# Kernel optimization log

Hardware: AMD Instinct MI355X
Metric: run time of the kernel (lower is better)

Reference implementation:

```python
import jax, jax.numpy as jnp
import numpy as np

B, S, D = 4, 2048, 1024
H, HD = 16, 64
DFF = 4096
EPS = 1e-6


def setup_inputs() -> dict:
    key = jax.random.key(0)
    ks = jax.random.split(key, 16)
    sc = 0.02
    def w(k, shape):
        return jax.random.normal(k, shape, dtype=jnp.float32) * sc
    return {
        'x': jax.random.normal(ks[0], (B, S, D), dtype=jnp.float32),
        'wq': w(ks[1], (D, D)), 'bq': jnp.zeros((D,), jnp.float32),
        'wk': w(ks[2], (D, D)), 'bk': jnp.zeros((D,), jnp.float32),
        'wv': w(ks[3], (D, D)), 'bv': jnp.zeros((D,), jnp.float32),
        'wo': w(ks[4], (D, D)), 'bo': jnp.zeros((D,), jnp.float32),
        'w1': w(ks[5], (D, DFF)), 'b1': jnp.zeros((DFF,), jnp.float32),
        'w2': w(ks[6], (DFF, D)), 'b2': jnp.zeros((D,), jnp.float32),
        'ln1_a': jnp.ones((D,), jnp.float32), 'ln1_b': jnp.zeros((D,), jnp.float32),
        'ln2_a': jnp.ones((D,), jnp.float32), 'ln2_b': jnp.zeros((D,), jnp.float32),
    }


def layernorm(x, alpha, bias):
    # Matches torch module: std is unbiased (ddof=1), divide by (std + eps)
    mean = jnp.mean(x, axis=-1, keepdims=True)
    var = jnp.sum((x - mean) ** 2, axis=-1, keepdims=True) / (x.shape[-1] - 1)
    std = jnp.sqrt(var)
    return alpha * ((x - mean) / (std + EPS)) + bias


def mha(x, wq, bq, wk, bk, wv, bv, wo, bo):
    q = (x @ wq + bq).reshape(B, S, H, HD)
    k = (x @ wk + bk).reshape(B, S, H, HD)
    v = (x @ wv + bv).reshape(B, S, H, HD)
    scores = jnp.einsum('bqhd,bkhd->bhqk', q, k) / jnp.sqrt(jnp.float32(HD))
    attn = jax.nn.softmax(scores, axis=-1)
    out = jnp.einsum('bhqk,bkhd->bqhd', attn, v).reshape(B, S, D)
    return out @ wo + bo


def reference(x, wq, bq, wk, bk, wv, bv, wo, bo, w1, b1, w2, b2,
              ln1_a, ln1_b, ln2_a, ln2_b):
    # Residual 1: x + MHA(LN(x))   (dropout = identity, eval mode)
    x = x + mha(layernorm(x, ln1_a, ln1_b), wq, bq, wk, bk, wv, bv, wo, bo)
    # Residual 2: x + FFN(LN(x))
    h = layernorm(x, ln2_a, ln2_b)
    ffn = jax.nn.relu(h @ w1 + b1) @ w2 + b2
    return x + ffn
```

## Files before the change

kernel.cpp:

```cpp
#include <hip/hip_runtime.h>

#define S_ 2048
#define D_ 1024

typedef unsigned short u16;
typedef unsigned int u32;
typedef __bf16 bf16x8 __attribute__((ext_vector_type(8)));
typedef unsigned short us8 __attribute__((ext_vector_type(8)));
typedef unsigned short us4 __attribute__((ext_vector_type(4)));
typedef unsigned int u32x4 __attribute__((ext_vector_type(4)));
typedef float f32x4 __attribute__((ext_vector_type(4)));

#if __has_builtin(__builtin_amdgcn_exp2f)
#define EXP2(x) __builtin_amdgcn_exp2f(x)
#else
#define EXP2(x) exp2f(x)
#endif

static __device__ __forceinline__ u16 f2bf(float f) {
  unsigned u = __builtin_bit_cast(unsigned, f);
  u += 0x7fffu + ((u >> 16) & 1u);
  return (u16)(u >> 16);
}

static __device__ __forceinline__ unsigned cvtpk_bf16(float lo, float hi) {
  unsigned r;
  asm("v_cvt_pk_bf16_f32 %0, %1, %2" : "=v"(r) : "v"(lo), "v"(hi));
  return r;
}

static __device__ __forceinline__ f32x4 mfma16(bf16x8 a, bf16x8 b, f32x4 c) {
  return __builtin_amdgcn_mfma_f32_16x16x32_bf16(a, b, c, 0, 0, 0);
}

static __device__ __forceinline__ void gload16(const void* g, void* lds) {
  __builtin_amdgcn_global_load_lds((const __attribute__((address_space(1))) void*)g,
                                   (__attribute__((address_space(3))) void*)lds, 16, 0, 0);
}

__global__ __launch_bounds__(256) void wtrans_kernel(const float* __restrict__ in,
                                                     u16* __restrict__ out, int K, int N,
                                                     float scale) {
  __shared__ float t[32][33];
  const int n0 = blockIdx.x * 32, k0 = blockIdx.y * 32;
  const int tx = threadIdx.x, ty = threadIdx.y;
#pragma unroll
  for (int i = 0; i < 4; i++)
    t[ty + 8 * i][tx] = in[(size_t)(k0 + ty + 8 * i) * N + n0 + tx];
  __syncthreads();
#pragma unroll
  for (int i = 0; i < 4; i++)
    out[(size_t)(n0 + ty + 8 * i) * K + k0 + tx] = f2bf(t[tx][ty + 8 * i] * scale);
}

__global__ __launch_bounds__(256) void bcat_kernel(const float* __restrict__ bq,
                                                   const float* __restrict__ bk,
                                                   const float* __restrict__ bv,
                                                   float* __restrict__ out, float qs) {
  const int i = blockIdx.x * 256 + threadIdx.x;
  out[i] = (i < 1024) ? bq[i] * qs : ((i < 2048) ? bk[i - 1024] : bv[i - 2048]);
}

__global__ __launch_bounds__(256) void ln_kernel(const float* __restrict__ in,
                                                 u16* __restrict__ out,
                                                 const float* __restrict__ alpha,
                                                 const float* __restrict__ beta) {
  const int row = blockIdx.x;
  const int tid = threadIdx.x;
  const float4 v = *(const float4*)(in + (size_t)row * D_ + tid * 4);
  float s = v.x + v.y + v.z + v.w;
  float ss = v.x * v.x + v.y * v.y + v.z * v.z + v.w * v.w;
#pragma unroll
  for (int off = 32; off >= 1; off >>= 1) {
    s += __shfl_xor(s, off);
    ss += __shfl_xor(ss, off);
  }
  __shared__ float red[8];
  const int w = tid >> 6, lane = tid & 63;
  if (lane == 0) { red[w] = s; red[4 + w] = ss; }
  __syncthreads();
  s = red[0] + red[1] + red[2] + red[3];
  ss = red[4] + red[5] + red[6] + red[7];
  const float mean = s * (1.0f / D_);
  const float var = (ss - s * mean) * (1.0f / (D_ - 1));
  const float inv = 1.0f / (sqrtf(var) + 1e-6f);
  const int j = tid * 4;
  const float4 av = *(const float4*)(alpha + j);
  const float4 bv = *(const float4*)(beta + j);
  us4 o;
  o[0] = f2bf((v.x - mean) * inv * av.x + bv.x);
  o[1] = f2bf((v.y - mean) * inv * av.y + bv.y);
  o[2] = f2bf((v.z - mean) * inv * av.z + bv.z);
  o[3] = f2bf((v.w - mean) * inv * av.w + bv.w);
  *(us4*)(out + (size_t)row * D_ + j) = o;
}

template <int OM, bool RELU, bool RESID>
__global__ __launch_bounds__(512, 2) void gemm_bt(const u16* __restrict__ A,
                                                  const u16* __restrict__ Bt,
                                                  const float* __restrict__ bias,
                                                  const float* __restrict__ resid,
                                                  void* __restrict__ outp,
                                                  void* __restrict__ out1,
                                                  void* __restrict__ out2, int N, int K) {
  __shared__ u16 lds[3 * 24576];
  const int tid = threadIdx.x;
  const int lane = tid & 63, w = tid >> 6;
  const int g = lane >> 4, r = lane & 15;
  const int wr = w >> 1, wc = w & 1;

  const int gx = gridDim.x;
  const int nwg = gx * gridDim.y;
  const int orig = blockIdx.y * gx + blockIdx.x;
  const int nid = (orig & 7) * (nwg >> 3) + (orig >> 3);
  const int bx = nid % gx, by = nid / gx;
  const size_t row0 = (size_t)by * 256;
  const int col0 = bx * 128;

  float bias4[4];
#pragma unroll
  for (int n = 0; n < 4; n++) bias4[n] = bias[col0 + wc * 64 + n * 16 + r];

  f32x4 acc[4][4];
#pragma unroll
  for (int m = 0; m < 4; m++)
#pragma unroll
    for (int n = 0; n < 4; n++) {
      f32x4 z = {bias4[n], bias4[n], bias4[n], bias4[n]};
      acc[m][n] = z;
    }

  const int lrow = w * 8 + (lane >> 3);
  const int scol = 8 * ((lane & 7) ^ (lane >> 3));
  const u16* gA = A + (row0 + lrow) * (size_t)K + scol;
  const u16* gB = Bt + ((size_t)col0 + lrow) * (size_t)K + scol;
  const int nt = K >> 6;
  const int sw = (r & 7) << 3;

  int bufi = 0;
#pragma unroll
  for (int t0 = 0; t0 < 2; t0++) {
    u16* dA = lds + t0 * 24576 + w * 512;
#pragma unroll
    for (int j = 0; j < 4; j++) gload16(gA + (size_t)(j * 64) * K + t0 * 64, dA + j * 4096);
#pragma unroll
    for (int j = 0; j < 2; j++)
      gload16(gB + (size_t)(j * 64) * K + t0 * 64, dA + 16384 + j * 4096);
  }

  for (int t = 0; t < nt; ++t) {
    if (t + 1 < nt)
      asm volatile("s_waitcnt vmcnt(6)" ::: "memory");
    else
      asm volatile("s_waitcnt vmcnt(0)" ::: "memory");
    __builtin_amdgcn_s_barrier();
    asm volatile("" ::: "memory");
    const bool st = (t + 2 < nt);
    const int bn = (bufi + 2 >= 3) ? bufi - 1 : bufi + 2;
    u16* dS = lds + bn * 24576 + w * 512;
    const size_t ko = (size_t)(t + 2) * 64;
    const u16* As_ = lds + bufi * 24576;
    const u16* Bs_ = As_ + 16384;
    bf16x8 bfr[2][4];

#pragma unroll
    for (int p = 0; p < 4; ++p) {
      bf16x8 a0 = __builtin_bit_cast(
          bf16x8, *(const us8*)(As_ + (wr * 64 + p * 16 + r) * 64 + ((g * 8) ^ sw)));
      bf16x8 a1 = __builtin_bit_cast(
          bf16x8, *(const us8*)(As_ + (wr * 64 + p * 16 + r) * 64 + ((32 + g * 8) ^ sw)));
      if (p == 0) {
#pragma unroll
        for (int kk = 0; kk < 2; kk++)
#pragma unroll
          for (int n = 0; n < 4; n++)
            bfr[kk][n] = __builtin_bit_cast(
                bf16x8,
                *(const us8*)(Bs_ + (wc * 64 + n * 16 + r) * 64 + ((kk * 32 + g * 8) ^ sw)));
      }
      if (st) {
        if (p == 0) {
          gload16(gA + ko, dS);
          gload16(gA + (size_t)64 * K + ko, dS + 4096);
        } else if (p == 1) {
          gload16(gA + (size_t)128 * K + ko, dS + 8192);
          gload16(gA + (size_t)192 * K + ko, dS + 12288);
        } else if (p == 2) {
          gload16(gB + ko, dS + 16384);
          gload16(gB + (size_t)64 * K + ko, dS + 20480);
        }
      }
      asm volatile("s_waitcnt lgkmcnt(0)" ::: "memory");
      __builtin_amdgcn_sched_barrier(0);
      __builtin_amdgcn_s_setprio(1);
#pragma unroll
      for (int n = 0; n < 4; n++) {
        acc[p][n] = mfma16(a0, bfr[0][n], acc[p][n]);
        acc[p][n] = mfma16(a1, bfr[1][n], acc[p][n]);
      }
      __builtin_amdgcn_s_setprio(0);
      if (p < 3) __builtin_amdgcn_s_barrier();
    }
    bufi = (bufi == 2) ? 0 : bufi + 1;
  }

#pragma unroll
  for (int m = 0; m < 4; m++)
#pragma unroll
    for (int n = 0; n < 4; n++) {
      if (OM == 2) {
        const int seg = col0 >> 10;
        const int cl = (col0 & 1023) + wc * 64 + n * 16 + r;
        if (seg == 2) {
          const int head = cl >> 6, hd = cl & 63;
          const size_t rg0 = row0 + wr * 64 + m * 16 + 4 * g;
          const int b = (int)(rg0 >> 11), s0 = (int)(rg0 & 2047);
          us4 o;
#pragma unroll
          for (int i = 0; i < 4; i++) o[i] = f2bf(acc[m][n][i]);
          *(us4*)((u16*)out2 + (((size_t)(b * 16 + head) * 64 + hd) * S_ + s0)) = o;
        } else {
          u16* dst = (u16*)(seg == 0 ? outp : out1);
#pragma unroll
          for (int i = 0; i < 4; i++) {
            const size_t rg = row0 + wr * 64 + m * 16 + 4 * g + i;
            dst[rg * D_ + cl] = f2bf(acc[m][n][i]);
          }
        }
      } else {
#pragma unroll
        for (int i = 0; i < 4; i++) {
          const size_t rg = row0 + wr * 64 + m * 16 + 4 * g + i;
          const int cg = col0 + wc * 64 + n * 16 + r;
          float v = acc[m][n][i];
          if (RESID) v += resid[rg * N + cg];
          if (RELU) v = fmaxf(v, 0.0f);
          if (OM == 1)
            ((float*)outp)[rg * N + cg] = v;
          else
            ((u16*)outp)[rg * N + cg] = f2bf(v);
        }
      }
    }
}

template <bool RELU>
__global__ __launch_bounds__(512, 2) void gemm_bt256(const u16* __restrict__ A,
                                                     const u16* __restrict__ Bt,
                                                     const float* __restrict__ bias,
                                                     u16* __restrict__ outp, int N, int K) {
  __shared__ u16 lds[2 * 32768];
  const int tid = threadIdx.x;
  const int lane = tid & 63, w = tid >> 6;
  const int g = lane >> 4, r = lane & 15;
  const int wr = w >> 2, wc = w & 3;
  const int gx = gridDim.x;
  const int nwg = gx * gridDim.y;
  const int orig = blockIdx.y * gx + blockIdx.x;
  const int nid = (orig & 7) * (nwg >> 3) + (orig >> 3);
  const int bx = nid % gx, by = nid / gx;
  const size_t row0 = (size_t)by * 256;
  const int col0 = bx * 256;

  float bias4[4];
#pragma unroll
  for (int n = 0; n < 4; n++) bias4[n] = bias[col0 + wc * 64 + n * 16 + r];

  f32x4 acc[8][4];
#pragma unroll
  for (int m = 0; m < 8; m++)
#pragma unroll
    for (int n = 0; n < 4; n++) {
      f32x4 z = {bias4[n], bias4[n], bias4[n], bias4[n]};
      acc[m][n] = z;
    }

  const int lrow = tid >> 3;
  const int scol = 8 * ((tid & 7) ^ (lrow & 7));
  const u16* gA = A + (row0 + lrow) * (size_t)K + scol;
  const u16* gB = Bt + ((size_t)col0 + lrow) * (size_t)K + scol;
  const int nt = K >> 6;
  const int sw = (r & 7) << 3;

  {
    u16* d = lds + w * 512;
#pragma unroll
    for (int j = 0; j < 4; j++) gload16(gA + (size_t)(j * 64) * K, d + j * 4096);
#pragma unroll
    for (int j = 0; j < 4; j++) gload16(gB + (size_t)(j * 64) * K, d + 16384 + j * 4096);
  }

  for (int t = 0; t < nt; ++t) {
    const u16* As_ = lds + (t & 1) * 32768;
    const u16* Bs_ = As_ + 16384;
    if (t + 1 < nt) {
      u16* d = lds + ((t + 1) & 1) * 32768 + w * 512;
      const size_t ko = (size_t)(t + 1) * 64;
#pragma unroll
      for (int j = 0; j < 4; j++) gload16(gA + (size_t)(j * 64) * K + ko, d + j * 4096);
#pragma unroll
      for (int j = 0; j < 4; j++) gload16(gB + (size_t)(j * 64) * K + ko, d + 16384 + j * 4096);
      asm volatile("s_waitcnt vmcnt(8)" ::: "memory");
    } else {
      asm volatile("s_waitcnt vmcnt(0)" ::: "memory");
    }
    __builtin_amdgcn_s_barrier();
    asm volatile("" ::: "memory");

    bf16x8 bfr[2][4];
#pragma unroll
    for (int kk = 0; kk < 2; kk++)
#pragma unroll
      for (int n = 0; n < 4; n++)
        bfr[kk][n] = __builtin_bit_cast(
            bf16x8, *(const us8*)(Bs_ + (wc * 64 + n * 16 + r) * 64 + ((kk * 32 + g * 8) ^ sw)));

#pragma unroll
    for (int p = 0; p < 4; ++p) {
      bf16x8 af[2][2];
#pragma unroll
      for (int mm = 0; mm < 2; mm++) {
        const int row = wr * 128 + (p * 2 + mm) * 16 + r;
        af[0][mm] = __builtin_bit_cast(bf16x8, *(const us8*)(As_ + row * 64 + ((g * 8) ^ sw)));
        af[1][mm] =
            __builtin_bit_cast(bf16x8, *(const us8*)(As_ + row * 64 + ((32 + g * 8) ^ sw)));
      }
      asm volatile("" ::: "memory");
      if (p > 0) __builtin_amdgcn_s_barrier();
      asm volatile("s_waitcnt lgkmcnt(0)" ::: "memory");
      __builtin_amdgcn_sched_barrier(0);
      __builtin_amdgcn_s_setprio(1);
#pragma unroll
      for (int mm = 0; mm < 2; mm++)
#pragma unroll
        for (int n = 0; n < 4; n++) {
          acc[p * 2 + mm][n] = mfma16(af[0][mm], bfr[0][n], acc[p * 2 + mm][n]);
          acc[p * 2 + mm][n] = mfma16(af[1][mm], bfr[1][n], acc[p * 2 + mm][n]);
        }
      __builtin_amdgcn_s_setprio(0);
    }
    asm volatile("" ::: "memory");
    __builtin_amdgcn_s_barrier();
  }

#pragma unroll
  for (int m = 0; m < 8; m++)
#pragma unroll
    for (int n = 0; n < 4; n++)
#pragma unroll
      for (int i = 0; i < 4; i++) {
        const size_t rg = row0 + wr * 128 + m * 16 + 4 * g + i;
        const int cg = col0 + wc * 64 + n * 16 + r;
        float v = acc[m][n][i];
        if (RELU) v = fmaxf(v, 0.0f);
        outp[rg * N + cg] = f2bf(v);
      }
}

__global__ __launch_bounds__(256) void attn_kernel(const u16* __restrict__ Q,
                                                   const u16* __restrict__ Km,
                                                   const u16* __restrict__ Vt_g,
                                                   u16* __restrict__ O) {
  __shared__ u16 Klds[64 * 64];
  __shared__ u16 Vlds[64 * 68];
  const int tid = threadIdx.x;
  const int lane = tid & 63, w = tid >> 6;
  const int g = lane >> 4, r = lane & 15;
  const int bh = blockIdx.y;
  const int b = bh >> 4, head = bh & 15;
  const size_t rowbase = (size_t)b * S_;
  const int colbase = head * 64;
  const int qw = blockIdx.x * 128 + w * 32;

  bf16x8 qf0[2], qf1[2];
#pragma unroll
  for (int qh = 0; qh < 2; qh++) {
    const u16* qrow = Q + (rowbase + qw + qh * 16 + r) * D_ + colbase;
    qf0[qh] = __builtin_bit_cast(bf16x8, *(const us8*)(qrow + g * 8));
    qf1[qh] = __builtin_bit_cast(bf16x8, *(const us8*)(qrow + 32 + g * 8));
  }

  const int srow = tid >> 3;
  const int sslot = (tid & 7) ^ (srow & 7);
  const u16* Kg = Km + (rowbase + srow) * D_ + colbase + sslot * 8;
  const u16* Vg = Vt_g + ((size_t)bh * 64 + srow) * S_ + (tid & 7) * 8;
  char* lK = (char*)Klds + w * 1024;

  const us8 onesw = {0x3F80, 0x3F80, 0x3F80, 0x3F80, 0x3F80, 0x3F80, 0x3F80, 0x3F80};
  const bf16x8 ones8 = __builtin_bit_cast(bf16x8, onesw);

  f32x4 lacc[2];
  f32x4 oacc[2][4];
#pragma unroll
  for (int qh = 0; qh < 2; qh++) {
    f32x4 z = {0.0f, 0.0f, 0.0f, 0.0f};
    lacc[qh] = z;
#pragma unroll
    for (int n = 0; n < 4; n++) oacc[qh][n] = z;
  }

  for (int kt = 0; kt < S_ / 64; kt++) {
    const us8 v0 = *(const us8*)(Vg + (size_t)kt * 64);
    const us8 v1 = *(const us8*)(Vg + 32 * S_ + (size_t)kt * 64);
    __syncthreads();
    gload16(Kg + (size_t)kt * 64 * D_, lK);
    gload16(Kg + (size_t)(kt * 64 + 32) * D_, lK + 4096);
    *(us8*)(Vlds + srow * 68 + (tid & 7) * 8) = v0;
    *(us8*)(Vlds + (srow + 32) * 68 + (tid & 7) * 8) = v1;
    __syncthreads();

    f32x4 st[4][2];
    __builtin_amdgcn_s_setprio(1);
#pragma unroll
    for (int f = 0; f < 4; f++) {
      const int row = f * 16 + r;
      const int sw = row & 7;
      const bf16x8 k0 = __builtin_bit_cast(bf16x8, *(const us8*)(Klds + row * 64 + (g ^ sw) * 8));
      const bf16x8 k1 =
          __builtin_bit_cast(bf16x8, *(const us8*)(Klds + row * 64 + ((g + 4) ^ sw) * 8));
#pragma unroll
      for (int qh = 0; qh < 2; qh++) {
        f32x4 z = {0.0f, 0.0f, 0.0f, 0.0f};
        st[f][qh] = mfma16(k0, qf0[qh], z);
        st[f][qh] = mfma16(k1, qf1[qh], st[f][qh]);
      }
    }
    __builtin_amdgcn_s_setprio(0);
    u32 pw[2][8];
#pragma unroll
    for (int qh = 0; qh < 2; qh++)
#pragma unroll
      for (int f = 0; f < 4; f++) {
        const float e0 = EXP2(st[f][qh][0]);
        const float e1 = EXP2(st[f][qh][1]);
        const float e2 = EXP2(st[f][qh][2]);
        const float e3 = EXP2(st[f][qh][3]);
        pw[qh][f * 2] = cvtpk_bf16(e0, e1);
        pw[qh][f * 2 + 1] = cvtpk_bf16(e2, e3);
      }

    bf16x8 a0[2], a1[2];
#pragma unroll
    for (int qh = 0; qh < 2; qh++) {
      const u32x4 a0w = {pw[qh][0], pw[qh][1], pw[qh][2], pw[qh][3]};
      const u32x4 a1w = {pw[qh][4], pw[qh][5], pw[qh][6], pw[qh][7]};
      a0[qh] = __builtin_bit_cast(bf16x8, a0w);
      a1[qh] = __builtin_bit_cast(bf16x8, a1w);
    }
    __builtin_amdgcn_s_setprio(1);
#pragma unroll
    for (int qh = 0; qh < 2; qh++) {
      lacc[qh] = mfma16(a0[qh], ones8, lacc[qh]);
      lacc[qh] = mfma16(a1[qh], ones8, lacc[qh]);
    }
#pragma unroll
    for (int n = 0; n < 4; n++) {
      const u16* vr = Vlds + (n * 16 + r) * 68;
      const us4 v00 = *(const us4*)(vr + g * 4);
      const us4 v01 = *(const us4*)(vr + 16 + g * 4);
      const us4 v10 = *(const us4*)(vr + 32 + g * 4);
      const us4 v11 = *(const us4*)(vr + 48 + g * 4);
      const bf16x8 vb0 =
          __builtin_bit_cast(bf16x8, __builtin_shufflevector(v00, v01, 0, 1, 2, 3, 4, 5, 6, 7));
      const bf16x8 vb1 =
          __builtin_bit_cast(bf16x8, __builtin_shufflevector(v10, v11, 0, 1, 2, 3, 4, 5, 6, 7));
#pragma unroll
      for (int qh = 0; qh < 2; qh++) {
        oacc[qh][n] = mfma16(a0[qh], vb0, oacc[qh][n]);
        oacc[qh][n] = mfma16(a1[qh], vb1, oacc[qh][n]);
      }
    }
    __builtin_amdgcn_s_setprio(0);
  }

#pragma unroll
  for (int qh = 0; qh < 2; qh++) {
    float ld[4];
#pragma unroll
    for (int i = 0; i < 4; i++) ld[i] = 1.0f / lacc[qh][i];
#pragma unroll
    for (int n = 0; n < 4; n++)
#pragma unroll
      for (int i = 0; i < 4; i++)
        O[(rowbase + qw + qh * 16 + 4 * g + i) * D_ + colbase + n * 16 + r] =
            f2bf(oacc[qh][n][i] * ld[i]);
  }
}

extern "C" void kernel_launch(void* const* d_in, const int* in_sizes, int n_in, void* d_out,
                              int out_size, void* d_ws, size_t ws_size, hipStream_t stream) {
  (void)in_sizes; (void)n_in; (void)out_size; (void)ws_size;
  const float* x = (const float*)d_in[0];
  const float* wq = (const float*)d_in[1];
  const float* bq = (const float*)d_in[2];
  const float* wk = (const float*)d_in[3];
  const float* bk = (const float*)d_in[4];
  const float* wv = (const float*)d_in[5];
  const float* bv = (const float*)d_in[6];
  const float* wo = (const float*)d_in[7];
  const float* bo = (const float*)d_in[8];
  const float* w1 = (const float*)d_in[9];
  const float* b1 = (const float*)d_in[10];
  const float* w2 = (const float*)d_in[11];
  const float* b2 = (const float*)d_in[12];
  const float* ln1a = (const float*)d_in[13];
  const float* ln1b = (const float*)d_in[14];
  const float* ln2a = (const float*)d_in[15];
  const float* ln2b = (const float*)d_in[16];

  char* ws = (char*)d_ws;
  const size_t MB = 1ull << 20;
  u16* wqkv = (u16*)(ws + 0 * MB);
  u16* wqt = wqkv;
  u16* wkt = (u16*)(ws + 2 * MB);
  u16* wvt = (u16*)(ws + 4 * MB);
  u16* wot = (u16*)(ws + 6 * MB);
  u16* w1t = (u16*)(ws + 8 * MB);
  u16* w2t = (u16*)(ws + 16 * MB);
  u16* xA = (u16*)(ws + 24 * MB);
  u16* qb = (u16*)(ws + 40 * MB);
  u16* kb = (u16*)(ws + 56 * MB);
  u16* vt = (u16*)(ws + 72 * MB);
  float* bcat = (float*)(ws + 88 * MB);
  u16* ff1 = (u16*)(ws + 40 * MB);
  float* x1 = (float*)(ws + 104 * MB);

  const float QSCALE = 0.125f * 1.4426950408889634f;

  const dim3 tb(32, 8);
  wtrans_kernel<<<dim3(32, 32), tb, 0, stream>>>(wq, wqt, 1024, 1024, QSCALE);
  wtrans_kernel<<<dim3(32, 32), tb, 0, stream>>>(wk, wkt, 1024, 1024, 1.0f);
  wtrans_kernel<<<dim3(32, 32), tb, 0, stream>>>(wv, wvt, 1024, 1024, 1.0f);
  wtrans_kernel<<<dim3(32, 32), tb, 0, stream>>>(wo, wot, 1024, 1024, 1.0f);
  wtrans_kernel<<<dim3(128, 32), tb, 0, stream>>>(w1, w1t, 1024, 4096, 1.0f);
  wtrans_kernel<<<dim3(32, 128), tb, 0, stream>>>(w2, w2t, 4096, 1024, 1.0f);
  bcat_kernel<<<12, 256, 0, stream>>>(bq, bk, bv, bcat, QSCALE);

  ln_kernel<<<8192, 256, 0, stream>>>(x, xA, ln1a, ln1b);
  gemm_bt<2, false, false><<<dim3(24, 32), 512, 0, stream>>>(xA, wqkv, bcat, nullptr, qb, kb, vt,
                                                             3072, 1024);
  attn_kernel<<<dim3(16, 64), 256, 0, stream>>>(qb, kb, vt, xA);
  gemm_bt<1, false, true><<<dim3(8, 32), 512, 0, stream>>>(xA, wot, bo, x, x1, nullptr, nullptr,
                                                           1024, 1024);
  ln_kernel<<<8192, 256, 0, stream>>>(x1, xA, ln2a, ln2b);
  gemm_bt256<true><<<dim3(16, 32), 512, 0, stream>>>(xA, w1t, b1, ff1, 4096, 1024);
  gemm_bt<1, false, true><<<dim3(8, 32), 512, 0, stream>>>(ff1, w2t, b2, x1, (float*)d_out,
                                                           nullptr, nullptr, 1024, 4096);
}
```

Before: 381.6 us.

## Double-buffer K/V tiles in attention and merge weight prep kernels

The attention kernel now double-buffers K and V tiles in LDS. The next tile's global loads are issued before the current tile's QK and PV MFMAs, and one barrier per iteration replaces two. Separately, the six weight-transpose launches and the bias-concat launch are folded into a single prep kernel to cut launch overhead. The cost is double the LDS use in attention, which may lower occupancy, plus a full vmcnt/lgkmcnt wait at the end of each iteration.

```diff
diff --git a/kernel.cpp b/kernel.cpp
--- a/kernel.cpp
+++ b/kernel.cpp
@@ -38,27 +38,44 @@
                                    (__attribute__((address_space(3))) void*)lds, 16, 0, 0);
 }
 
-__global__ __launch_bounds__(256) void wtrans_kernel(const float* __restrict__ in,
-                                                     u16* __restrict__ out, int K, int N,
-                                                     float scale) {
+__global__ __launch_bounds__(256) void prep_kernel(
+    const float* __restrict__ wq, const float* __restrict__ wk, const float* __restrict__ wv,
+    const float* __restrict__ wo, const float* __restrict__ w1, const float* __restrict__ w2,
+    const float* __restrict__ bq, const float* __restrict__ bk, const float* __restrict__ bv,
+    u16* __restrict__ wqkv, u16* __restrict__ wot, u16* __restrict__ w1t,
+    u16* __restrict__ w2t, float* __restrict__ bcat, float qs) {
+  const int bid = blockIdx.x;
+  const int tx = threadIdx.x, ty = threadIdx.y;
+  if (bid >= 12288) {
+    const int i = (bid - 12288) * 256 + ty * 32 + tx;
+    bcat[i] = (i < 1024) ? bq[i] * qs : ((i < 2048) ? bk[i - 1024] : bv[i - 2048]);
+    return;
+  }
+  const float* in;
+  u16* out;
+  int K, N, idx;
+  float sc = 1.0f;
+  if (bid < 4096) {
+    K = 1024; N = 1024; idx = bid & 1023;
+    if (bid < 1024)      { in = wq; out = wqkv;             sc = qs; }
+    else if (bid < 2048) { in = wk; out = wqkv + (1 << 20); }
+    else if (bid < 3072) { in = wv; out = wqkv + (2 << 20); }
+    else                 { in = wo; out = wot; }
+  } else if (bid < 8192) {
+    in = w1; out = w1t; K = 1024; N = 4096; idx = bid - 4096;
+  } else {
+    in = w2; out = w2t; K = 4096; N = 1024; idx = bid - 8192;
+  }
+  const int nb = N >> 5;
+  const int n0 = (idx % nb) * 32, k0 = (idx / nb) * 32;
   __shared__ float t[32][33];
-  const int n0 = blockIdx.x * 32, k0 = blockIdx.y * 32;
-  const int tx = threadIdx.x, ty = threadIdx.y;
 #pragma unroll
   for (int i = 0; i < 4; i++)
     t[ty + 8 * i][tx] = in[(size_t)(k0 + ty + 8 * i) * N + n0 + tx];
   __syncthreads();
 #pragma unroll
   for (int i = 0; i < 4; i++)
-    out[(size_t)(n0 + ty + 8 * i) * K + k0 + tx] = f2bf(t[tx][ty + 8 * i] * scale);
-}
-
-__global__ __launch_bounds__(256) void bcat_kernel(const float* __restrict__ bq,
-                                                   const float* __restrict__ bk,
-                                                   const float* __restrict__ bv,
-                                                   float* __restrict__ out, float qs) {
-  const int i = blockIdx.x * 256 + threadIdx.x;
-  out[i] = (i < 1024) ? bq[i] * qs : ((i < 2048) ? bk[i - 1024] : bv[i - 2048]);
+    out[(size_t)(n0 + ty + 8 * i) * K + k0 + tx] = f2bf(t[tx][ty + 8 * i] * sc);
 }
 
 __global__ __launch_bounds__(256) void ln_kernel(const float* __restrict__ in,
@@ -361,8 +378,8 @@
                                                    const u16* __restrict__ Km,
                                                    const u16* __restrict__ Vt_g,
                                                    u16* __restrict__ O) {
-  __shared__ u16 Klds[64 * 64];
-  __shared__ u16 Vlds[64 * 68];
+  __shared__ u16 Klds[2 * 4096];
+  __shared__ u16 Vlds[2 * 4352];
   const int tid = threadIdx.x;
   const int lane = tid & 63, w = tid >> 6;
   const int g = lane >> 4, r = lane & 15;
@@ -384,7 +401,6 @@
   const int sslot = (tid & 7) ^ (srow & 7);
   const u16* Kg = Km + (rowbase + srow) * D_ + colbase + sslot * 8;
   const u16* Vg = Vt_g + ((size_t)bh * 64 + srow) * S_ + (tid & 7) * 8;
-  char* lK = (char*)Klds + w * 1024;
 
   const us8 onesw = {0x3F80, 0x3F80, 0x3F80, 0x3F80, 0x3F80, 0x3F80, 0x3F80, 0x3F80};
   const bf16x8 ones8 = __builtin_bit_cast(bf16x8, onesw);
@@ -399,15 +415,29 @@
     for (int n = 0; n < 4; n++) oacc[qh][n] = z;
   }
 
+  {
+    const us8 pv0 = *(const us8*)(Vg);
+    const us8 pv1 = *(const us8*)(Vg + 32 * S_);
+    gload16(Kg, (char*)Klds + w * 1024);
+    gload16(Kg + (size_t)32 * D_, (char*)Klds + w * 1024 + 4096);
+    *(us8*)(Vlds + srow * 68 + (tid & 7) * 8) = pv0;
+    *(us8*)(Vlds + (srow + 32) * 68 + (tid & 7) * 8) = pv1;
+    __syncthreads();
+  }
+
   for (int kt = 0; kt < S_ / 64; kt++) {
-    const us8 v0 = *(const us8*)(Vg + (size_t)kt * 64);
-    const us8 v1 = *(const us8*)(Vg + 32 * S_ + (size_t)kt * 64);
-    __syncthreads();
-    gload16(Kg + (size_t)kt * 64 * D_, lK);
-    gload16(Kg + (size_t)(kt * 64 + 32) * D_, lK + 4096);
-    *(us8*)(Vlds + srow * 68 + (tid & 7) * 8) = v0;
-    *(us8*)(Vlds + (srow + 32) * 68 + (tid & 7) * 8) = v1;
-    __syncthreads();
+    const int cur = kt & 1, nxt = cur ^ 1;
+    const bool more = (kt + 1 < S_ / 64);
+    us8 nv0, nv1;
+    if (more) {
+      nv0 = *(const us8*)(Vg + (size_t)(kt + 1) * 64);
+      nv1 = *(const us8*)(Vg + 32 * S_ + (size_t)(kt + 1) * 64);
+      gload16(Kg + (size_t)(kt + 1) * 64 * D_, (char*)Klds + nxt * 8192 + w * 1024);
+      gload16(Kg + (size_t)((kt + 1) * 64 + 32) * D_,
+              (char*)Klds + nxt * 8192 + w * 1024 + 4096);
+    }
+    const u16* Kc = Klds + cur * 4096;
+    const u16* Vc = Vlds + cur * 4352;
 
     f32x4 st[4][2];
     __builtin_amdgcn_s_setprio(1);
@@ -415,9 +445,9 @@
     for (int f = 0; f < 4; f++) {
       const int row = f * 16 + r;
       const int sw = row & 7;
-      const bf16x8 k0 = __builtin_bit_cast(bf16x8, *(const us8*)(Klds + row * 64 + (g ^ sw) * 8));
+      const bf16x8 k0 = __builtin_bit_cast(bf16x8, *(const us8*)(Kc + row * 64 + (g ^ sw) * 8));
       const bf16x8 k1 =
-          __builtin_bit_cast(bf16x8, *(const us8*)(Klds + row * 64 + ((g + 4) ^ sw) * 8));
+          __builtin_bit_cast(bf16x8, *(const us8*)(Kc + row * 64 + ((g + 4) ^ sw) * 8));
 #pragma unroll
       for (int qh = 0; qh < 2; qh++) {
         f32x4 z = {0.0f, 0.0f, 0.0f, 0.0f};
@@ -438,6 +468,10 @@
         pw[qh][f * 2] = cvtpk_bf16(e0, e1);
         pw[qh][f * 2 + 1] = cvtpk_bf16(e2, e3);
       }
+    if (more) {
+      *(us8*)(Vlds + nxt * 4352 + srow * 68 + (tid & 7) * 8) = nv0;
+      *(us8*)(Vlds + nxt * 4352 + (srow + 32) * 68 + (tid & 7) * 8) = nv1;
+    }
 
     bf16x8 a0[2], a1[2];
 #pragma unroll
@@ -455,7 +489,7 @@
     }
 #pragma unroll
     for (int n = 0; n < 4; n++) {
-      const u16* vr = Vlds + (n * 16 + r) * 68;
+      const u16* vr = Vc + (n * 16 + r) * 68;
       const us4 v00 = *(const us4*)(vr + g * 4);
       const us4 v01 = *(const us4*)(vr + 16 + g * 4);
       const us4 v10 = *(const us4*)(vr + 32 + g * 4);
@@ -471,6 +505,9 @@
       }
     }
     __builtin_amdgcn_s_setprio(0);
+    asm volatile("s_waitcnt vmcnt(0) lgkmcnt(0)" ::: "memory");
+    __builtin_amdgcn_s_barrier();
+    asm volatile("" ::: "memory");
   }
 
 #pragma unroll
@@ -511,9 +548,6 @@
   char* ws = (char*)d_ws;
   const size_t MB = 1ull << 20;
   u16* wqkv = (u16*)(ws + 0 * MB);
-  u16* wqt = wqkv;
-  u16* wkt = (u16*)(ws + 2 * MB);
-  u16* wvt = (u16*)(ws + 4 * MB);
   u16* wot = (u16*)(ws + 6 * MB);
   u16* w1t = (u16*)(ws + 8 * MB);
   u16* w2t = (u16*)(ws + 16 * MB);
@@ -527,14 +561,8 @@
 
   const float QSCALE = 0.125f * 1.4426950408889634f;
 
-  const dim3 tb(32, 8);
-  wtrans_kernel<<<dim3(32, 32), tb, 0, stream>>>(wq, wqt, 1024, 1024, QSCALE);
-  wtrans_kernel<<<dim3(32, 32), tb, 0, stream>>>(wk, wkt, 1024, 1024, 1.0f);
-  wtrans_kernel<<<dim3(32, 32), tb, 0, stream>>>(wv, wvt, 1024, 1024, 1.0f);
-  wtrans_kernel<<<dim3(32, 32), tb, 0, stream>>>(wo, wot, 1024, 1024, 1.0f);
-  wtrans_kernel<<<dim3(128, 32), tb, 0, stream>>>(w1, w1t, 1024, 4096, 1.0f);
-  wtrans_kernel<<<dim3(32, 128), tb, 0, stream>>>(w2, w2t, 4096, 1024, 1.0f);
-  bcat_kernel<<<12, 256, 0, stream>>>(bq, bk, bv, bcat, QSCALE);
+  prep_kernel<<<12300, dim3(32, 8), 0, stream>>>(wq, wk, wv, wo, w1, w2, bq, bk, bv, wqkv, wot,
+                                                 w1t, w2t, bcat, QSCALE);
 
   ln_kernel<<<8192, 256, 0, stream>>>(x, xA, ln1a, ln1b);
   gemm_bt<2, false, false><<<dim3(24, 32), 512, 0, stream>>>(xA, wqkv, bcat, nullptr, qb, kb, vt,
```

After: 370.5 us. 2.9% less time.
